# Kernel optimization log

Measured on AMD Instinct MI355X. Metric: run time of the kernel, lower is better.

Reference implementation:

```python
import jax, jax.numpy as jnp
import numpy as np

N_NODES = 100000
N_EDGES = 1600000
D_IN = 128
D_H = 128
N_CLASSES = 64


def setup_inputs() -> dict:
    key = jax.random.key(0)
    ks = jax.random.split(key, 8)
    feat = jax.random.normal(ks[0], (N_NODES, D_IN), dtype=jnp.float32)
    src = jax.random.randint(ks[1], (N_EDGES,), 0, N_NODES)
    dst = jax.random.randint(ks[2], (N_EDGES,), 0, N_NODES)
    # Xavier-ish scaled weights (nn.Linear layout: [out, in])
    W1 = jax.random.normal(ks[3], (D_H, D_IN), dtype=jnp.float32) * (1.0 / np.sqrt(D_IN))
    b1 = jnp.zeros((D_H,), dtype=jnp.float32)
    W2 = jax.random.normal(ks[4], (D_H, D_H), dtype=jnp.float32) * (1.0 / np.sqrt(D_H))
    b2 = jnp.zeros((D_H,), dtype=jnp.float32)
    Wl = jax.random.normal(ks[5], (N_CLASSES, 2 * D_H), dtype=jnp.float32) * (1.0 / np.sqrt(2 * D_H))
    bl = jnp.zeros((N_CLASSES,), dtype=jnp.float32)
    return {"feat": feat, "src": src, "dst": dst, "W1": W1, "b1": b1,
            "W2": W2, "b2": b2, "Wl": Wl, "bl": bl}


def _mean_agg(h, src, dst, inv_deg, n):
    # copy_u('h','m') + mean('m','neigh'): gather src features, segment-sum on dst, divide by in-degree
    s = jax.ops.segment_sum(h[src], dst, num_segments=n)  # [N, D]
    return s * inv_deg


def reference(feat, src, dst, W1, b1, W2, b2, Wl, bl):
    n = feat.shape[0]
    deg = jax.ops.segment_sum(jnp.ones_like(dst, dtype=feat.dtype), dst, num_segments=n)
    inv_deg = (1.0 / jnp.maximum(deg, 1.0))[:, None]  # zero-degree nodes -> 0 (sum is 0 anyway)
    h1 = jax.nn.relu(_mean_agg(feat, src, dst, inv_deg, n) @ W1.T + b1)
    h2 = jax.nn.relu(_mean_agg(h1, src, dst, inv_deg, n) @ W2.T + b2)
    logits = jnp.concatenate([h1, h2], axis=-1) @ Wl.T + bl
    return jax.nn.log_softmax(logits, axis=-1)
```

## Files before the change

### kernel.cpp

```cpp
#include <hip/hip_runtime.h>
#include <stdint.h>

#define D 128
#define NCLS 64
#define BSH 8
#define BNODES 256
#define BMASK 255
#define NBMAX 1024
#define CCHUNK 4096
#define HISTB 256
#define GEMMB 2048

typedef __bf16 bf16x8 __attribute__((ext_vector_type(8)));
typedef float f32x4 __attribute__((ext_vector_type(4)));
typedef float f32x2 __attribute__((ext_vector_type(2)));

union B8 { uint4 u; bf16x8 v; };

__device__ __forceinline__ B8 pack8(const float4& a, const float4& b) {
  union { __bf16 h[8]; uint4 u; } p;
  p.h[0] = (__bf16)a.x; p.h[1] = (__bf16)a.y; p.h[2] = (__bf16)a.z; p.h[3] = (__bf16)a.w;
  p.h[4] = (__bf16)b.x; p.h[5] = (__bf16)b.y; p.h[6] = (__bf16)b.z; p.h[7] = (__bf16)b.w;
  B8 r; r.u = p.u; return r;
}

__device__ __forceinline__ void store_fp8_rows(unsigned char* __restrict__ Z,
                                               const f32x4& acc, int row0, int col, int N) {
  const int p01 = __builtin_amdgcn_cvt_pk_fp8_f32(acc[0], acc[1], 0, false);
  const int p23 = __builtin_amdgcn_cvt_pk_fp8_f32(acc[2], acc[3], 0, false);
  const unsigned char b0 = (unsigned char)(p01 & 0xff);
  const unsigned char b1 = (unsigned char)((p01 >> 8) & 0xff);
  const unsigned char b2 = (unsigned char)(p23 & 0xff);
  const unsigned char b3 = (unsigned char)((p23 >> 8) & 0xff);
  if (row0 + 0 < N) Z[(size_t)(row0 + 0) * D + col] = b0;
  if (row0 + 1 < N) Z[(size_t)(row0 + 1) * D + col] = b1;
  if (row0 + 2 < N) Z[(size_t)(row0 + 2) * D + col] = b2;
  if (row0 + 3 < N) Z[(size_t)(row0 + 3) * D + col] = b3;
}


__global__ __launch_bounds__(256) void k_pre(const int* __restrict__ dst,
                                             const float* __restrict__ feat,
                                             const float* __restrict__ W1,
                                             int* __restrict__ bcnt,
                                             unsigned char* __restrict__ Z,
                                             int N, int E, int NB) {
  __shared__ int h[NBMAX];
  if (blockIdx.x < HISTB) {
    for (int i = threadIdx.x; i < NB; i += 256) h[i] = 0;
    __syncthreads();
    for (int e = blockIdx.x * 256 + threadIdx.x; e < E; e += HISTB * 256)
      atomicAdd(&h[dst[e] >> BSH], 1);
    __syncthreads();
    for (int i = threadIdx.x; i < NB; i += 256) {
      int c = h[i];
      if (c) atomicAdd(&bcnt[i], c);
    }
    return;
  }
  const int bid = blockIdx.x - HISTB;
  const int wave = threadIdx.x >> 6;
  const int lane = threadIdx.x & 63;
  const int l15 = lane & 15;
  const int quad = lane >> 4;

  B8 bfrag[2][4];
#pragma unroll
  for (int t = 0; t < 2; ++t) {
    const int n = wave * 32 + t * 16 + l15;
    const float* wp = W1 + (size_t)n * D + quad * 8;
#pragma unroll
    for (int ks = 0; ks < 4; ++ks)
      bfrag[t][ks] = pack8(*reinterpret_cast<const float4*>(wp + ks * 32),
                           *reinterpret_cast<const float4*>(wp + ks * 32 + 4));
  }

  const int mtiles = (N + 15) >> 4;
  for (int mt = bid; mt < mtiles; mt += GEMMB) {
    const int arow = min(mt * 16 + l15, N - 1);
    const float* ap = feat + (size_t)arow * D + quad * 8;
    B8 a[4];
#pragma unroll
    for (int ks = 0; ks < 4; ++ks)
      a[ks] = pack8(*reinterpret_cast<const float4*>(ap + ks * 32),
                    *reinterpret_cast<const float4*>(ap + ks * 32 + 4));
#pragma unroll
    for (int t = 0; t < 2; ++t) {
      f32x4 acc = {0.f, 0.f, 0.f, 0.f};
#pragma unroll
      for (int ks = 0; ks < 4; ++ks)
        acc = __builtin_amdgcn_mfma_f32_16x16x32_bf16(a[ks].v, bfrag[t][ks].v, acc, 0, 0, 0);
      store_fp8_rows(Z, acc, mt * 16 + quad * 4, wave * 32 + t * 16 + l15, N);
    }
  }
}


__global__ __launch_bounds__(1024) void k_bscan(const int* __restrict__ bcnt,
                                                int* __restrict__ bbase,
                                                int* __restrict__ bcur, int NB, int E) {
  __shared__ int sm[NBMAX];
  const int tid = threadIdx.x;
  int v = (tid < NB) ? bcnt[tid] : 0;
  sm[tid] = v;
  __syncthreads();
  for (int off = 1; off < NBMAX; off <<= 1) {
    int t = (tid >= off) ? sm[tid - off] : 0;
    __syncthreads();
    sm[tid] += t;
    __syncthreads();
  }
  if (tid < NB) {
    bbase[tid] = sm[tid] - v;
    bcur[tid] = sm[tid] - v;
  }
  if (tid == 0) bbase[NB] = E;
}

__global__ __launch_bounds__(256) void k_bscatter(const int* __restrict__ src,
                                                  const int* __restrict__ dst,
                                                  int* __restrict__ bcur,
                                                  int* __restrict__ ebuck, int E, int NB) {
  __shared__ int h[NBMAX];
  __shared__ int base[NBMAX];
  const int tid = threadIdx.x;
  const int beg = blockIdx.x * CCHUNK;
  const int end = min(beg + CCHUNK, E);
  int d[16];
#pragma unroll
  for (int i = 0; i < 16; ++i) {
    const int e = beg + i * 256 + tid;
    d[i] = (e < end) ? dst[e] : -1;
  }
  for (int i = tid; i < NB; i += 256) h[i] = 0;
  __syncthreads();
#pragma unroll
  for (int i = 0; i < 16; ++i)
    if (d[i] >= 0) atomicAdd(&h[d[i] >> BSH], 1);
  __syncthreads();
  for (int i = tid; i < NB; i += 256) {
    const int c = h[i];
    base[i] = c ? atomicAdd(&bcur[i], c) : 0;
    h[i] = 0;
  }
  __syncthreads();
#pragma unroll
  for (int i = 0; i < 16; ++i) {
    if (d[i] >= 0) {
      const int e = beg + i * 256 + tid;
      const int b = d[i] >> BSH;
      const int r = atomicAdd(&h[b], 1);
      ebuck[base[b] + r] = (src[e] << BSH) | (d[i] & BMASK);
    }
  }
}

__global__ __launch_bounds__(256) void k_bbuild(const int* __restrict__ ebuck,
                                                const int* __restrict__ bbase,
                                                int* __restrict__ row_ptr,
                                                int* __restrict__ esrc,
                                                float* __restrict__ inv, int N, int E) {
  __shared__ int cnt[BNODES], s[BNODES], cur[BNODES];
  const int b = blockIdx.x;
  const int n0 = b << BSH;
  const int nn = min(BNODES, N - n0);
  const int beg = bbase[b], end = bbase[b + 1];
  const int tid = threadIdx.x;
  int v[16];
#pragma unroll
  for (int i = 0; i < 16; ++i) {
    const int e = beg + i * 256 + tid;
    v[i] = (e < end) ? ebuck[e] : -1;
  }
  cnt[tid] = 0;
  __syncthreads();
#pragma unroll
  for (int i = 0; i < 16; ++i)
    if (v[i] >= 0) atomicAdd(&cnt[v[i] & BMASK], 1);
  for (int e = beg + 4096 + tid; e < end; e += 256)
    atomicAdd(&cnt[ebuck[e] & BMASK], 1);
  __syncthreads();
  s[tid] = cnt[tid];
  __syncthreads();
  for (int off = 1; off < BNODES; off <<= 1) {
    const int t = (tid >= off) ? s[tid - off] : 0;
    __syncthreads();
    s[tid] += t;
    __syncthreads();
  }
  {
    const int ex = s[tid] - cnt[tid];
    cur[tid] = ex;
    if (tid < nn) {
      row_ptr[n0 + tid] = beg + ex;
      inv[n0 + tid] = 1.0f / fmaxf((float)cnt[tid], 1.0f);
    }
  }
  if (b == 0 && tid == 0) row_ptr[N] = E;
  __syncthreads();
#pragma unroll
  for (int i = 0; i < 16; ++i)
    if (v[i] >= 0) {
      const int r = atomicAdd(&cur[v[i] & BMASK], 1);
      esrc[beg + r] = v[i] >> BSH;
    }
  for (int e = beg + 4096 + tid; e < end; e += 256) {
    const int p = ebuck[e];
    const int r = atomicAdd(&cur[p & BMASK], 1);
    esrc[beg + r] = p >> BSH;
  }
}


__global__ __launch_bounds__(256) void k_gemmz2(const ushort* __restrict__ A,
                                                const float* __restrict__ W,
                                                unsigned char* __restrict__ Z, int N) {
  const int wave = threadIdx.x >> 6;
  const int lane = threadIdx.x & 63;
  const int l15 = lane & 15;
  const int quad = lane >> 4;

  B8 bfrag[2][4];
#pragma unroll
  for (int t = 0; t < 2; ++t) {
    const int n = wave * 32 + t * 16 + l15;
    const float* wp = W + (size_t)n * D + quad * 8;
#pragma unroll
    for (int ks = 0; ks < 4; ++ks)
      bfrag[t][ks] = pack8(*reinterpret_cast<const float4*>(wp + ks * 32),
                           *reinterpret_cast<const float4*>(wp + ks * 32 + 4));
  }

  const int mtiles = (N + 15) >> 4;
  for (int mt = blockIdx.x; mt < mtiles; mt += gridDim.x) {
    const int arow = min(mt * 16 + l15, N - 1);
    const ushort* ap = A + (size_t)arow * D + quad * 8;
    B8 a[4];
#pragma unroll
    for (int ks = 0; ks < 4; ++ks)
      a[ks].u = *reinterpret_cast<const uint4*>(ap + ks * 32);
#pragma unroll
    for (int t = 0; t < 2; ++t) {
      f32x4 acc = {0.f, 0.f, 0.f, 0.f};
#pragma unroll
      for (int ks = 0; ks < 4; ++ks)
        acc = __builtin_amdgcn_mfma_f32_16x16x32_bf16(a[ks].v, bfrag[t][ks].v, acc, 0, 0, 0);
      store_fp8_rows(Z, acc, mt * 16 + quad * 4, wave * 32 + t * 16 + l15, N);
    }
  }
}


__device__ __forceinline__ void accq8pk(f32x2 acc[4], const uint2& u) {
  acc[0] += __builtin_amdgcn_cvt_pk_f32_fp8((int)u.x, false);
  acc[1] += __builtin_amdgcn_cvt_pk_f32_fp8((int)u.x, true);
  acc[2] += __builtin_amdgcn_cvt_pk_f32_fp8((int)u.y, false);
  acc[3] += __builtin_amdgcn_cvt_pk_f32_fp8((int)u.y, true);
}

__device__ __forceinline__ void gather_acc8(const unsigned char* __restrict__ hp,
                                            const int* __restrict__ esrc,
                                            int beg, int end, f32x2 acc[4]) {
  const int n4 = (end - beg) >> 2;
  int e = beg;
  if (n4 > 0) {
    int4 ss = *reinterpret_cast<const int4*>(esrc + e);
    for (int it = 0; it < n4; ++it) {
      const uint2 u0 = *reinterpret_cast<const uint2*>(hp + (size_t)ss.x * D);
      const uint2 u1 = *reinterpret_cast<const uint2*>(hp + (size_t)ss.y * D);
      const uint2 u2 = *reinterpret_cast<const uint2*>(hp + (size_t)ss.z * D);
      const uint2 u3 = *reinterpret_cast<const uint2*>(hp + (size_t)ss.w * D);
      e += 4;
      if (it + 1 < n4) ss = *reinterpret_cast<const int4*>(esrc + e);
      accq8pk(acc, u0);
      accq8pk(acc, u1);
      accq8pk(acc, u2);
      accq8pk(acc, u3);
    }
  }
  for (; e < end; ++e) {
    const uint2 u0 = *reinterpret_cast<const uint2*>(hp + (size_t)esrc[e] * D);
    accq8pk(acc, u0);
  }
}


__global__ __launch_bounds__(256) void k_gather_relu(const unsigned char* __restrict__ z,
                                                     const int* __restrict__ row_ptr,
                                                     const int* __restrict__ esrc,
                                                     const float* __restrict__ inv,
                                                     const float* __restrict__ bias,
                                                     ushort* __restrict__ out, int N) {
  const int g = threadIdx.x >> 4;
  const int w = threadIdx.x & 15;
  const unsigned char* hp = z + w * 8;
  float bb[8];
  {
    const float4 x = *reinterpret_cast<const float4*>(bias + w * 8);
    const float4 y = *reinterpret_cast<const float4*>(bias + w * 8 + 4);
    bb[0] = x.x; bb[1] = x.y; bb[2] = x.z; bb[3] = x.w;
    bb[4] = y.x; bb[5] = y.y; bb[6] = y.z; bb[7] = y.w;
  }
  const int ntiles = (N + 15) >> 4;
  for (int tile = blockIdx.x; tile < ntiles; tile += gridDim.x) {
    const int node = tile * 16 + g;
    if (node >= N) continue;
    f32x2 acc[4] = {{0.f, 0.f}, {0.f, 0.f}, {0.f, 0.f}, {0.f, 0.f}};
    gather_acc8(hp, esrc, row_ptr[node], row_ptr[node + 1], acc);
    const float iv = inv[node];
    union { __bf16 b[8]; uint4 u; } p;
#pragma unroll
    for (int i = 0; i < 4; ++i) {
      p.b[i * 2 + 0] = (__bf16)fmaxf(acc[i].x * iv + bb[i * 2 + 0], 0.f);
      p.b[i * 2 + 1] = (__bf16)fmaxf(acc[i].y * iv + bb[i * 2 + 1], 0.f);
    }
    *reinterpret_cast<uint4*>(out + (size_t)node * D + w * 8) = p.u;
  }
}


__global__ __launch_bounds__(256, 2) void k_logits(const ushort* __restrict__ h1,
                                                   const ushort* __restrict__ h2,
                                                   const float* __restrict__ Wl,
                                                   const float* __restrict__ bl,
                                                   float* __restrict__ out, int N) {
  const int lane = threadIdx.x & 63;
  const int l15 = lane & 15;
  const int quad = lane >> 4;
  const int wid = blockIdx.x * 4 + (threadIdx.x >> 6);
  const int nw = gridDim.x * 4;

  B8 wfrag[4][8];
  float blv[4];
#pragma unroll
  for (int t = 0; t < 4; ++t) {
    const int n = t * 16 + l15;
    blv[t] = bl[n];
    const float* wp = Wl + (size_t)n * (2 * D) + quad * 8;
#pragma unroll
    for (int ks = 0; ks < 8; ++ks)
      wfrag[t][ks] = pack8(*reinterpret_cast<const float4*>(wp + ks * 32),
                           *reinterpret_cast<const float4*>(wp + ks * 32 + 4));
  }

  const int mtiles = (N + 15) >> 4;
  for (int mt = wid; mt < mtiles; mt += nw) {
    const int arow = min(mt * 16 + l15, N - 1);
    const ushort* p1 = h1 + (size_t)arow * D + quad * 8;
    const ushort* p2 = h2 + (size_t)arow * D + quad * 8;
    B8 a1[4], a2[4];
#pragma unroll
    for (int ks = 0; ks < 4; ++ks) {
      a1[ks].u = *reinterpret_cast<const uint4*>(p1 + ks * 32);
      a2[ks].u = *reinterpret_cast<const uint4*>(p2 + ks * 32);
    }
    f32x4 acc[4];
#pragma unroll
    for (int t = 0; t < 4; ++t) acc[t] = f32x4{0.f, 0.f, 0.f, 0.f};
#pragma unroll
    for (int ks = 0; ks < 4; ++ks)
#pragma unroll
      for (int t = 0; t < 4; ++t)
        acc[t] = __builtin_amdgcn_mfma_f32_16x16x32_bf16(a1[ks].v, wfrag[t][ks].v, acc[t], 0, 0, 0);
#pragma unroll
    for (int ks = 0; ks < 4; ++ks)
#pragma unroll
      for (int t = 0; t < 4; ++t)
        acc[t] = __builtin_amdgcn_mfma_f32_16x16x32_bf16(a2[ks].v, wfrag[t][4 + ks].v, acc[t], 0, 0, 0);
#pragma unroll
    for (int t = 0; t < 4; ++t)
#pragma unroll
      for (int r = 0; r < 4; ++r)
        acc[t][r] += blv[t];
#pragma unroll
    for (int r = 0; r < 4; ++r) {
      float m = fmaxf(fmaxf(acc[0][r], acc[1][r]), fmaxf(acc[2][r], acc[3][r]));
#pragma unroll
      for (int off = 8; off > 0; off >>= 1) m = fmaxf(m, __shfl_xor(m, off));
      const float e0 = __expf(acc[0][r] - m);
      const float e1 = __expf(acc[1][r] - m);
      const float e2 = __expf(acc[2][r] - m);
      const float e3 = __expf(acc[3][r] - m);
      float s = (e0 + e1) + (e2 + e3);
#pragma unroll
      for (int off = 8; off > 0; off >>= 1) s += __shfl_xor(s, off);
      const float ls = m + __logf(s);
      const int orow = mt * 16 + quad * 4 + r;
      if (orow < N) {
        float* op = out + (size_t)orow * NCLS + l15;
#pragma unroll
        for (int t = 0; t < 4; ++t) op[t * 16] = acc[t][r] - ls;
      }
    }
  }
}


extern "C" void kernel_launch(void* const* d_in, const int* in_sizes, int n_in,
                              void* d_out, int out_size, void* d_ws, size_t ws_size,
                              hipStream_t stream) {
  const float* feat = (const float*)d_in[0];
  const int* src = (const int*)d_in[1];
  const int* dst = (const int*)d_in[2];
  const float* W1 = (const float*)d_in[3];
  const float* b1 = (const float*)d_in[4];
  const float* W2 = (const float*)d_in[5];
  const float* b2 = (const float*)d_in[6];
  const float* Wl = (const float*)d_in[7];
  const float* bl = (const float*)d_in[8];
  float* out = (float*)d_out;

  const int N = in_sizes[0] / D;
  const int E = in_sizes[1];
  const int NB = (N + BNODES - 1) >> BSH;

  float* ws = (float*)d_ws;
  float* inv = ws;
  ushort* h1b = (ushort*)(inv + N);
  ushort* h2b = h1b + (size_t)N * D;
  unsigned char* z8 = (unsigned char*)(h2b + (size_t)N * D);
  int* row_ptr = (int*)(z8 + (size_t)N * D);
  int* esrc = row_ptr + N + 1;
  int* ebuck = esrc + E;
  int* bcnt = ebuck + E;
  int* bbase = bcnt + NBMAX;
  int* bcur = bbase + NBMAX + 1;

  hipMemsetAsync(bcnt, 0, NBMAX * sizeof(int), stream);

  k_pre<<<HISTB + GEMMB, 256, 0, stream>>>(dst, feat, W1, bcnt, z8, N, E, NB);

  k_bscan<<<1, 1024, 0, stream>>>(bcnt, bbase, bcur, NB, E);
  k_bscatter<<<(E + CCHUNK - 1) / CCHUNK, 256, 0, stream>>>(src, dst, bcur, ebuck, E, NB);
  k_bbuild<<<NB, 256, 0, stream>>>(ebuck, bbase, row_ptr, esrc, inv, N, E);

  k_gather_relu<<<2048, 256, 0, stream>>>(z8, row_ptr, esrc, inv, b1, h1b, N);

  k_gemmz2<<<2048, 256, 0, stream>>>(h1b, W2, z8, N);
  k_gather_relu<<<2048, 256, 0, stream>>>(z8, row_ptr, esrc, inv, b2, h2b, N);

  k_logits<<<512, 256, 0, stream>>>(h1b, h2b, Wl, bl, out, N);
}
```

Before: 316.9 us.

## Split first-layer GEMM across scatter and bucket-build kernels to overlap CSR construction

Moves the feat·W1ᵀ GEMM out of the histogram kernel and splits its M-tiles (4/7 and 3/7) across the bucket-scatter and bucket-build kernels as extra blocks. The histogram now runs alone, and the GEMM work co-runs with the atomic-heavy CSR construction stages, so compute and memory-latency-bound graph preprocessing share the device. It keeps the same kernel count but adds fixed block-count and split-ratio tuning, and the histogram kernel loses its former overlap with the GEMM.

```diff
diff --git a/kernel.cpp b/kernel.cpp
--- a/kernel.cpp
+++ b/kernel.cpp
@@ -9,7 +9,8 @@
 #define NBMAX 1024
 #define CCHUNK 4096
 #define HISTB 256
-#define GEMMB 2048
+#define GB1 1664
+#define GB2 1664
 
 typedef __bf16 bf16x8 __attribute__((ext_vector_type(8)));
 typedef float f32x4 __attribute__((ext_vector_type(4)));
@@ -39,28 +40,13 @@
 }
 
 
-__global__ __launch_bounds__(256) void k_pre(const int* __restrict__ dst,
-                                             const float* __restrict__ feat,
-                                             const float* __restrict__ W1,
-                                             int* __restrict__ bcnt,
-                                             unsigned char* __restrict__ Z,
-                                             int N, int E, int NB) {
-  __shared__ int h[NBMAX];
-  if (blockIdx.x < HISTB) {
-    for (int i = threadIdx.x; i < NB; i += 256) h[i] = 0;
-    __syncthreads();
-    for (int e = blockIdx.x * 256 + threadIdx.x; e < E; e += HISTB * 256)
-      atomicAdd(&h[dst[e] >> BSH], 1);
-    __syncthreads();
-    for (int i = threadIdx.x; i < NB; i += 256) {
-      int c = h[i];
-      if (c) atomicAdd(&bcnt[i], c);
-    }
-    return;
-  }
-  const int bid = blockIdx.x - HISTB;
-  const int wave = threadIdx.x >> 6;
-  const int lane = threadIdx.x & 63;
+__device__ __forceinline__ void gemm_z1_range(const float* __restrict__ feat,
+                                              const float* __restrict__ W1,
+                                              unsigned char* __restrict__ Z,
+                                              int N, int t0, int t1,
+                                              int bid, int nblk, int tid) {
+  const int wave = tid >> 6;
+  const int lane = tid & 63;
   const int l15 = lane & 15;
   const int quad = lane >> 4;
 
@@ -75,8 +61,7 @@
                            *reinterpret_cast<const float4*>(wp + ks * 32 + 4));
   }
 
-  const int mtiles = (N + 15) >> 4;
-  for (int mt = bid; mt < mtiles; mt += GEMMB) {
+  for (int mt = t0 + bid; mt < t1; mt += nblk) {
     const int arow = min(mt * 16 + l15, N - 1);
     const float* ap = feat + (size_t)arow * D + quad * 8;
     B8 a[4];
@@ -95,6 +80,20 @@
   }
 }
 
+
+__global__ __launch_bounds__(256) void k_hist(const int* __restrict__ dst,
+                                              int* __restrict__ bcnt, int E, int NB) {
+  __shared__ int h[NBMAX];
+  for (int i = threadIdx.x; i < NB; i += 256) h[i] = 0;
+  __syncthreads();
+  for (int e = blockIdx.x * 256 + threadIdx.x; e < E; e += HISTB * 256)
+    atomicAdd(&h[dst[e] >> BSH], 1);
+  __syncthreads();
+  for (int i = threadIdx.x; i < NB; i += 256) {
+    int c = h[i];
+    if (c) atomicAdd(&bcnt[i], c);
+  }
+}
 
 __global__ __launch_bounds__(1024) void k_bscan(const int* __restrict__ bcnt,
                                                 int* __restrict__ bbase,
@@ -117,13 +116,22 @@
   if (tid == 0) bbase[NB] = E;
 }
 
-__global__ __launch_bounds__(256) void k_bscatter(const int* __restrict__ src,
-                                                  const int* __restrict__ dst,
-                                                  int* __restrict__ bcur,
-                                                  int* __restrict__ ebuck, int E, int NB) {
+
+__global__ __launch_bounds__(256) void k_sg1(const int* __restrict__ src,
+                                             const int* __restrict__ dst,
+                                             int* __restrict__ bcur,
+                                             int* __restrict__ ebuck,
+                                             const float* __restrict__ feat,
+                                             const float* __restrict__ W1,
+                                             unsigned char* __restrict__ Z,
+                                             int N, int E, int NB, int scb, int t1) {
   __shared__ int h[NBMAX];
   __shared__ int base[NBMAX];
   const int tid = threadIdx.x;
+  if ((int)blockIdx.x >= scb) {
+    gemm_z1_range(feat, W1, Z, N, 0, t1, blockIdx.x - scb, GB1, tid);
+    return;
+  }
   const int beg = blockIdx.x * CCHUNK;
   const int end = min(beg + CCHUNK, E);
   int d[16];
@@ -155,17 +163,27 @@
   }
 }
 
-__global__ __launch_bounds__(256) void k_bbuild(const int* __restrict__ ebuck,
-                                                const int* __restrict__ bbase,
-                                                int* __restrict__ row_ptr,
-                                                int* __restrict__ esrc,
-                                                float* __restrict__ inv, int N, int E) {
+
+__global__ __launch_bounds__(256) void k_bg2(const int* __restrict__ ebuck,
+                                             const int* __restrict__ bbase,
+                                             int* __restrict__ row_ptr,
+                                             int* __restrict__ esrc,
+                                             float* __restrict__ inv,
+                                             const float* __restrict__ feat,
+                                             const float* __restrict__ W1,
+                                             unsigned char* __restrict__ Z,
+                                             int N, int E, int NB, int t1) {
   __shared__ int cnt[BNODES], s[BNODES], cur[BNODES];
+  const int tid = threadIdx.x;
+  if ((int)blockIdx.x >= NB) {
+    const int mtiles = (N + 15) >> 4;
+    gemm_z1_range(feat, W1, Z, N, t1, mtiles, blockIdx.x - NB, GB2, tid);
+    return;
+  }
   const int b = blockIdx.x;
   const int n0 = b << BSH;
   const int nn = min(BNODES, N - n0);
   const int beg = bbase[b], end = bbase[b + 1];
-  const int tid = threadIdx.x;
   int v[16];
 #pragma unroll
   for (int i = 0; i < 16; ++i) {
@@ -413,6 +431,9 @@
   const int N = in_sizes[0] / D;
   const int E = in_sizes[1];
   const int NB = (N + BNODES - 1) >> BSH;
+  const int SCB = (E + CCHUNK - 1) / CCHUNK;
+  const int mtiles = (N + 15) >> 4;
+  const int T1 = (mtiles * 4) / 7;
 
   float* ws = (float*)d_ws;
   float* inv = ws;
@@ -428,11 +449,12 @@
 
   hipMemsetAsync(bcnt, 0, NBMAX * sizeof(int), stream);
 
-  k_pre<<<HISTB + GEMMB, 256, 0, stream>>>(dst, feat, W1, bcnt, z8, N, E, NB);
-
+  k_hist<<<HISTB, 256, 0, stream>>>(dst, bcnt, E, NB);
   k_bscan<<<1, 1024, 0, stream>>>(bcnt, bbase, bcur, NB, E);
-  k_bscatter<<<(E + CCHUNK - 1) / CCHUNK, 256, 0, stream>>>(src, dst, bcur, ebuck, E, NB);
-  k_bbuild<<<NB, 256, 0, stream>>>(ebuck, bbase, row_ptr, esrc, inv, N, E);
+  k_sg1<<<SCB + GB1, 256, 0, stream>>>(src, dst, bcur, ebuck, feat, W1, z8,
+                                       N, E, NB, SCB, T1);
+  k_bg2<<<NB + GB2, 256, 0, stream>>>(ebuck, bbase, row_ptr, esrc, inv,
+                                      feat, W1, z8, N, E, NB, T1);
 
   k_gather_relu<<<2048, 256, 0, stream>>>(z8, row_ptr, esrc, inv, b1, h1b, N);
 
```

Measured after the change: 331.3 us. 4.5% more time.
